# Performance work log

Hardware: AMD Instinct MI355X
Metric: run time of the kernel (lower is better)

The kernel has to match this reference:

```python
import jax, jax.numpy as jnp
import numpy as np
from jax.scipy.special import gammaln

NEARZERO = 1e-5
LENF = 15  # gamma unit-hydrograph length (days)

# (name, low, high) in the exact order of Exphydro.parameter_bounds
PHY_BOUNDS = [
    ('ddf', 0.0, 40.0), ('Tbm', -2.0, 3.0), ('wrf', 0.0, 0.5), ('Tbf', -5.0, 2.0),
    ('Kf', 0.0, 5.0), ('exp_fe', 0.0, 1.0), ('ET_efficiency', 0.0, 1.0),
    ('coef_runoff', 0.0, 1.0), ('coef_vadose2phreatic', 1e-5, 0.02),
    ('coef_vadose', 0.0, 0.1), ('coef_phreatic', 1e-5, 0.01),
    ('vadose_max_level', 1e-3, 500.0)]
ROUT_BOUNDS = [('alpha1', 0.3, 20.0), ('beta1', 0.01, 5.0),
               ('alpha2', 0.5, 13.0), ('beta2', 0.15, 1.5)]


def setup_inputs() -> dict:
    key = jax.random.key(0)
    k1, k2, k3, k4 = jax.random.split(key, 4)
    T, G = 1095, 15000
    prcp = jax.random.uniform(k1, (T, G), dtype=jnp.float32) * 10.0   # mm/day
    tmean = jax.random.normal(k2, (T, G), dtype=jnp.float32) * 10.0   # deg C (spans <0 and >0)
    pet = jax.random.uniform(k3, (T, G), dtype=jnp.float32) * 5.0     # mm/day
    x_phy = jnp.stack([prcp, tmean, pet], axis=-1)                    # [T, G, 3]
    params = jax.random.uniform(k4, (G, 16), dtype=jnp.float32)       # normalized in [0,1]
    return {'x_phy': x_phy, 'params': params}


def _descale(p, lo, hi):
    # change_param_range: linear rescale of [0,1]-normalized params
    return p * (hi - lo) + lo


def _uh_gamma(alpha, theta, lenF=LENF):
    # Gamma-pdf unit hydrograph, normalized. alpha, theta: [G] -> w: [lenF, G]
    t = jnp.arange(lenF, dtype=alpha.dtype) + 0.5          # midpoint of each day
    a = alpha[None, :]
    th = theta[None, :]
    logw = (a - 1.0) * jnp.log(t[:, None]) - t[:, None] / th - gammaln(a) - a * jnp.log(th)
    w = jnp.exp(logw)
    return w / jnp.sum(w, axis=0, keepdims=True)


def _uh_conv(q, w):
    # causal depthwise convolution along time. q: [T, G], w: [L, G]
    T = q.shape[0]
    L = w.shape[0]
    qp = jnp.pad(q, ((L - 1, 0), (0, 0)))
    out = jnp.zeros_like(q)
    for l in range(L):  # fixed small L=15, unrolled at trace time
        out = out + w[l][None, :] * qp[L - 1 - l:L - 1 - l + T]
    return out


def _forward(x_phy, params):
    G = params.shape[0]
    # unpack + descale: 12 static physical params [G,1] (nmul=1), 4 routing params [G]
    phy = {name: _descale(params[:, i:i + 1], lo, hi)
           for i, (name, lo, hi) in enumerate(PHY_BOUNDS)}
    rout = {name: _descale(params[:, 12 + i], lo, hi)
            for i, (name, lo, hi) in enumerate(ROUT_BOUNDS)}

    P = x_phy[..., 0:1]    # [T, G, 1] precip
    Tm = x_phy[..., 1:2]   # [T, G, 1] mean temperature
    Pet = x_phy[..., 2:3]  # [T, G, 1] potential ET

    def step(carry, inp):
        sog, wis, vad, phr = carry  # snow-on-ground, water-in-snowpack, vadose, phreatic [G,1]
        p, tm, pet = inp
        rain = p * (tm >= 0.0).astype(p.dtype)
        snow = p * (tm < 0.0).astype(p.dtype)
        # overnight refreezing of liquid water in snowpack
        pot_freeze = phy['Kf'] * jnp.clip(phy['Tbf'] - tm, NEARZERO, None) ** phy['exp_fe']
        freeze = jnp.minimum(pot_freeze, wis)
        wis = wis - freeze
        sog = sog + freeze
        # degree-day snowmelt
        melt = jnp.minimum(jnp.clip(phy['ddf'] * (tm - phy['Tbm']), 0.0, None), sog + snow)
        sog = sog + snow - melt
        # snowpack liquid retention
        retention = phy['wrf'] * sog
        wtmp = wis + melt + rain
        avail = jnp.clip(wtmp - retention, 0.0, None)
        wis = jnp.where(avail > 0.0, retention, wtmp)
        # soil buckets
        ret_pot = phy['ET_efficiency'] * pet
        ratio = vad / phy['vadose_max_level']
        ht0 = phy['coef_runoff'] * ratio * avail                 # surface runoff
        infil = avail - ht0
        ht1 = phy['coef_vadose2phreatic'] * ratio * vad          # vadose -> phreatic
        ht2 = phy['coef_vadose'] * vad                           # delayed runoff (interflow)
        ht3 = phy['coef_phreatic'] * phr                         # baseflow
        aet = jnp.minimum(ret_pot, vad)                          # actual ET
        vad = vad + infil - aet - ht1 - ht2
        overflow = jnp.clip(vad - phy['vadose_max_level'], 0.0, None)
        vad = jnp.clip(vad, NEARZERO, phy['vadose_max_level'])
        ht0 = ht0 + overflow
        phr = jnp.clip(phr + ht1 - ht3, NEARZERO, None)
        return (sog, wis, vad, phr), (ht0, ht2, ht3, aet, vad, phr)

    init = tuple(jnp.full((G, 1), NEARZERO, dtype=x_phy.dtype) for _ in range(4))
    _, (ht0, ht2, ht3, aet, vad_sim, phr_sim) = jax.lax.scan(step, init, (P, Tm, Pet))

    # average over nmul (muwts=None, nmul=1) -> [T, G]
    q_surf = jnp.mean(ht0, axis=-1)
    q_delay = jnp.mean(ht2 + ht3, axis=-1)
    # gamma unit-hydrograph routing
    uh1 = _uh_gamma(rout['alpha1'], rout['beta1'])
    uh2 = _uh_gamma(rout['alpha2'], rout['beta2'])
    return _uh_conv(q_surf, uh1) + _uh_conv(q_delay, uh2)  # streamflow [T, G]


def reference(x_phy, params):
    return _forward(x_phy, params)
```

## Files before the change

kernel.cpp:

```cpp
#include <hip/hip_runtime.h>

#define LENF 15
#define NZ   1e-5f

typedef float f32x2 __attribute__((ext_vector_type(2)));

struct R3 { float p, t, e; };

__global__ __launch_bounds__(64, 1) void exphydro_kernel(
    const float* __restrict__ x,
    const float* __restrict__ params,
    float* __restrict__ out,
    int G, int T)
{
  int g = blockIdx.x * 64 + threadIdx.x;
  if (g >= G) return;

  const float* pp = params + (size_t)g * 16;
  float P0[16];
#pragma unroll
  for (int i = 0; i < 16; ++i) P0[i] = pp[i];

  const float ddf    = P0[0]  * 40.f;
  const float Tbm    = P0[1]  * 5.f  - 2.f;
  const float wrf    = P0[2]  * 0.5f;
  const float Tbf    = P0[3]  * 7.f  - 5.f;
  const float Kf     = P0[4]  * 5.f;
  const float exp_fe = P0[5];
  const float ET_eff = P0[6];
  const float c_vad  = P0[9]  * 0.1f;
  const float c_phr  = P0[10] * (0.01f - 1e-5f) + 1e-5f;
  const float vml    = P0[11] * (500.f - 0.001f) + 0.001f;
  const float inv_vml = 1.f / vml;
  const float crp    = P0[7] * inv_vml;
  const float cvp    = (P0[8] * (0.02f - 1e-5f) + 1e-5f) * inv_vml;
  const float mpb    = ddf * Tbm;
  const float a1     = P0[12] * (20.f - 0.3f)  + 0.3f;
  const float b1     = P0[13] * (5.f  - 0.01f) + 0.01f;
  const float a2     = P0[14] * (13.f - 0.5f)  + 0.5f;
  const float b2     = P0[15] * (1.5f - 0.15f) + 0.15f;

  f32x2 wv[LENF];
  {
    float lw1[LENF], lw2[LENF];
    float m1 = -1e30f, m2 = -1e30f;
    const float ib1 = 1.f / b1, ib2 = 1.f / b2;
#pragma unroll
    for (int l = 0; l < LENF; ++l) {
      float tt = l + 0.5f;
      float lt = __logf(tt);
      lw1[l] = (a1 - 1.f) * lt - tt * ib1;
      lw2[l] = (a2 - 1.f) * lt - tt * ib2;
      m1 = fmaxf(m1, lw1[l]);
      m2 = fmaxf(m2, lw2[l]);
    }
    float s1 = 0.f, s2 = 0.f;
    float t1[LENF], t2[LENF];
#pragma unroll
    for (int l = 0; l < LENF; ++l) {
      t1[l] = __expf(lw1[l] - m1); s1 += t1[l];
      t2[l] = __expf(lw2[l] - m2); s2 += t2[l];
    }
    const float r1 = 1.f / s1, r2 = 1.f / s2;
#pragma unroll
    for (int l = 0; l < LENF; ++l) { wv[l].x = t1[l] * r1; wv[l].y = t2[l] * r2; }
  }

  float sog = NZ, wis = NZ, vad = NZ, phr = NZ;
  f32x2 D[LENF - 1];
#pragma unroll
  for (int l = 0; l < LENF - 1; ++l) D[l] = (f32x2){0.f, 0.f};

  const unsigned Gu = (unsigned)G;
  const R3* xg = (const R3*)x + g;
  unsigned oof = (unsigned)g;

  R3 A[LENF], B[LENF];
  float pf[LENF], mp[LENF], rp[LENF];

  const int nb   = T / LENF;
  const int tail = T - nb * LENF;

#define LOAD(BUF, blk)                                                \
  {                                                                   \
    unsigned b0_ = (unsigned)(blk) * (unsigned)LENF * Gu;             \
    _Pragma("unroll")                                                 \
    for (int j = 0; j < LENF; ++j) BUF[j] = xg[b0_ + (unsigned)j * Gu]; \
  }

#define PREP(BUF)                                                     \
  {                                                                   \
    _Pragma("unroll")                                                 \
    for (int j = 0; j < LENF; ++j) {                                  \
      float tm_ = BUF[j].t;                                           \
      pf[j] = Kf * __builtin_amdgcn_exp2f(                            \
                  exp_fe * __builtin_amdgcn_logf(fmaxf(Tbf - tm_, NZ))); \
      mp[j] = fmaxf(ddf * tm_ - mpb, 0.f);                            \
      rp[j] = ET_eff * BUF[j].e;                                      \
    }                                                                 \
  }

#define STEP(BUF, I_)                                                 \
  {                                                                   \
    float p_ = BUF[I_].p, tm_ = BUF[I_].t;                            \
    float rain = (tm_ >= 0.f) ? p_ : 0.f;                             \
    float snow = p_ - rain;                                           \
    float freeze = fminf(pf[I_], wis);                                \
    wis -= freeze;                                                    \
    float sos = sog + freeze + snow;                                  \
    float melt = fminf(mp[I_], sos);                                  \
    sog = sos - melt;                                                 \
    float ret = wrf * sog;                                            \
    float wtmp = wis + melt + rain;                                   \
    float avail = fmaxf(wtmp - ret, 0.f);                             \
    wis = fminf(wtmp, ret);              \
    float t1_ = crp * vad;                                            \
    float ht0 = t1_ * avail;                                          \
    float t2_ = cvp * vad;                                            \
    float ht1 = t2_ * vad;                                            \
    float ht2 = c_vad * vad;                                          \
    float ht3 = c_phr * phr;                                          \
    float infil = avail - ht0;                                        \
    float aet = fminf(rp[I_], vad);                                   \
    float va_ = vad + infil;                                          \
    float vb_ = aet + ht1;                                            \
    float v2_ = va_ - vb_ - ht2;                                      \
    float overflow = fmaxf(v2_ - vml, 0.f);                           \
    vad = fminf(fmaxf(v2_, NZ), vml);                 \
    float qx = ht0 + overflow;                                        \
    phr = fmaxf(phr + ht1 - ht3, NZ);                                 \
    f32x2 q_; q_.x = qx; q_.y = ht2 + ht3;                            \
    f32x2 o_ = D[0] + wv[0] * q_;                                     \
    _Pragma("unroll")                                                 \
    for (int l = 0; l < LENF - 2; ++l)                                \
      D[l] = D[l + 1] + wv[l + 1] * q_;             \
    D[LENF - 2] = wv[LENF - 1] * q_;                                  \
    out[oof] = o_.x + o_.y;                                           \
    oof += Gu;                                                        \
  }

#define BLOCK(BUF)                                                    \
  {                                                                   \
    PREP(BUF);                                                        \
    _Pragma("unroll")                                                 \
    for (int i = 0; i < LENF; ++i) STEP(BUF, i);                      \
  }

  if (nb > 0) LOAD(A, 0);

  int k = 0;
  while (k + 2 <= nb) {
    LOAD(B, k + 1);
    BLOCK(A);
    if (k + 2 < nb) LOAD(A, k + 2);
    BLOCK(B);
    k += 2;
  }
  if (k < nb) {
    BLOCK(A);
  }
  if (tail > 0) {
    unsigned b0 = (unsigned)nb * (unsigned)LENF * Gu;
    for (int j = 0; j < tail; ++j) {
      A[0] = xg[b0 + (unsigned)j * Gu];
      float tm_ = A[0].t;
      pf[0] = Kf * __builtin_amdgcn_exp2f(
                  exp_fe * __builtin_amdgcn_logf(fmaxf(Tbf - tm_, NZ)));
      mp[0] = fmaxf(ddf * tm_ - mpb, 0.f);
      rp[0] = ET_eff * A[0].e;
      STEP(A, 0);
    }
  }

#undef LOAD
#undef PREP
#undef STEP
#undef BLOCK
}

extern "C" void kernel_launch(void* const* d_in, const int* in_sizes, int n_in,
                              void* d_out, int out_size, void* d_ws, size_t ws_size,
                              hipStream_t stream) {
  const float* x      = (const float*)d_in[0];
  const float* params = (const float*)d_in[1];
  float* out          = (float*)d_out;

  int G = in_sizes[1] / 16;
  int T = in_sizes[0] / (G * 3);

  int block = 64;
  int grid  = (G + block - 1) / block;
  exphydro_kernel<<<grid, block, 0, stream>>>(x, params, out, G, T);
}
```

Before: 149.5 us.

## Software-pipeline snow and soil phases across time chunks to expose ILP

Splits each serial time step into a snow/melt phase and a soil/routing phase. The soil phase of chunk k-1 is interleaved with the snow phase of chunk k, which are independent, so the latency-bound recurrence has two dependency chains in flight. It also cuts the input chunk from 15 to 5 steps, double-buffered, and replaces the tail path with clamped loads and guarded counts. The shorter prefetch distance may hide memory latency less well, and the extra avail/rp arrays add register pressure.

```diff
diff --git a/kernel.cpp b/kernel.cpp
--- a/kernel.cpp
+++ b/kernel.cpp
@@ -1,6 +1,7 @@
 #include <hip/hip_runtime.h>
 
 #define LENF 15
+#define BLK  5
 #define NZ   1e-5f
 
 typedef float f32x2 __attribute__((ext_vector_type(2)));
@@ -66,7 +67,8 @@
     for (int l = 0; l < LENF; ++l) { wv[l].x = t1[l] * r1; wv[l].y = t2[l] * r2; }
   }
 
-  float sog = NZ, wis = NZ, vad = NZ, phr = NZ;
+  float sog = NZ, wis = NZ;
+  float vad = NZ, phr = NZ;
   f32x2 D[LENF - 1];
 #pragma unroll
   for (int l = 0; l < LENF - 1; ++l) D[l] = (f32x2){0.f, 0.f};
@@ -74,57 +76,67 @@
   const unsigned Gu = (unsigned)G;
   const R3* xg = (const R3*)x + g;
   unsigned oof = (unsigned)g;
-
-  R3 A[LENF], B[LENF];
-  float pf[LENF], mp[LENF], rp[LENF];
-
-  const int nb   = T / LENF;
-  const int tail = T - nb * LENF;
-
-#define LOAD(BUF, blk)                                                \
-  {                                                                   \
-    unsigned b0_ = (unsigned)(blk) * (unsigned)LENF * Gu;             \
-    _Pragma("unroll")                                                 \
-    for (int j = 0; j < LENF; ++j) BUF[j] = xg[b0_ + (unsigned)j * Gu]; \
-  }
-
-#define PREP(BUF)                                                     \
-  {                                                                   \
-    _Pragma("unroll")                                                 \
-    for (int j = 0; j < LENF; ++j) {                                  \
-      float tm_ = BUF[j].t;                                           \
-      pf[j] = Kf * __builtin_amdgcn_exp2f(                            \
-                  exp_fe * __builtin_amdgcn_logf(fmaxf(Tbf - tm_, NZ))); \
-      mp[j] = fmaxf(ddf * tm_ - mpb, 0.f);                            \
-      rp[j] = ET_eff * BUF[j].e;                                      \
+  const unsigned tmax = (unsigned)(T - 1);
+
+  R3 XA[BLK], XB[BLK];
+  float pf[BLK], mp[BLK];
+  float avail[BLK], rp[BLK];
+
+  const int nc = (T + BLK - 1) / BLK;
+
+#define LOADC(BUF, c)                                                 \
+  {                                                                   \
+    unsigned tb_ = (unsigned)(c) * (unsigned)BLK;                     \
+    _Pragma("unroll")                                                 \
+    for (int j = 0; j < BLK; ++j) {                                   \
+      unsigned t_ = tb_ + (unsigned)j;                                \
+      if (t_ > tmax) t_ = tmax;                                       \
+      BUF[j] = xg[t_ * Gu];                                           \
     }                                                                 \
   }
 
-#define STEP(BUF, I_)                                                 \
-  {                                                                   \
-    float p_ = BUF[I_].p, tm_ = BUF[I_].t;                            \
+#define PREPC(BUF, cnt)                                               \
+  {                                                                   \
+    _Pragma("unroll")                                                 \
+    for (int j = 0; j < BLK; ++j) {                                   \
+      if (j < (cnt)) {                                                \
+        float tm_ = BUF[j].t;                                         \
+        pf[j] = Kf * __builtin_amdgcn_exp2f(                          \
+            exp_fe * __builtin_amdgcn_logf(fmaxf(Tbf - tm_, NZ)));    \
+        mp[j] = fmaxf(ddf * tm_ - mpb, 0.f);                          \
+      }                                                               \
+    }                                                                 \
+  }
+
+#define P1STEP(BUF, J_)                                               \
+  {                                                                   \
+    float p_ = BUF[J_].p, tm_ = BUF[J_].t;                            \
     float rain = (tm_ >= 0.f) ? p_ : 0.f;                             \
     float snow = p_ - rain;                                           \
-    float freeze = fminf(pf[I_], wis);                                \
+    float freeze = fminf(pf[J_], wis);                                \
     wis -= freeze;                                                    \
     float sos = sog + freeze + snow;                                  \
-    float melt = fminf(mp[I_], sos);                                  \
+    float melt = fminf(mp[J_], sos);                                  \
     sog = sos - melt;                                                 \
     float ret = wrf * sog;                                            \
     float wtmp = wis + melt + rain;                                   \
-    float avail = fmaxf(wtmp - ret, 0.f);                             \
+    avail[J_] = fmaxf(wtmp - ret, 0.f);                               \
     wis = fminf(wtmp, ret);              \
+    rp[J_] = ET_eff * BUF[J_].e;                                      \
+  }
+
+#define P2STEP(J_)                                                    \
+  {                                                                   \
+    float av_ = avail[J_], rp_ = rp[J_];                              \
     float t1_ = crp * vad;                                            \
-    float ht0 = t1_ * avail;                                          \
+    float ht0 = t1_ * av_;                                            \
     float t2_ = cvp * vad;                                            \
     float ht1 = t2_ * vad;                                            \
     float ht2 = c_vad * vad;                                          \
     float ht3 = c_phr * phr;                                          \
-    float infil = avail - ht0;                                        \
-    float aet = fminf(rp[I_], vad);                                   \
-    float va_ = vad + infil;                                          \
-    float vb_ = aet + ht1;                                            \
-    float v2_ = va_ - vb_ - ht2;                                      \
+    float infil = av_ - ht0;                                          \
+    float aet = fminf(rp_, vad);                                      \
+    float v2_ = vad + infil - aet - ht1 - ht2;                        \
     float overflow = fmaxf(v2_ - vml, 0.f);                           \
     vad = fminf(fmaxf(v2_, NZ), vml);                 \
     float qx = ht0 + overflow;                                        \
@@ -139,43 +151,52 @@
     oof += Gu;                                                        \
   }
 
-#define BLOCK(BUF)                                                    \
-  {                                                                   \
-    PREP(BUF);                                                        \
-    _Pragma("unroll")                                                 \
-    for (int i = 0; i < LENF; ++i) STEP(BUF, i);                      \
-  }
-
-  if (nb > 0) LOAD(A, 0);
-
-  int k = 0;
-  while (k + 2 <= nb) {
-    LOAD(B, k + 1);
-    BLOCK(A);
-    if (k + 2 < nb) LOAD(A, k + 2);
-    BLOCK(B);
+#define CHUNK(BUF, p1cnt, p2cnt)                                      \
+  {                                                                   \
+    PREPC(BUF, p1cnt);                                                \
+    _Pragma("unroll")                                                 \
+    for (int j = 0; j < BLK; ++j) {                                   \
+      if (j < (p2cnt)) P2STEP(j);                                     \
+      if (j < (p1cnt)) P1STEP(BUF, j);                                \
+    }                                                                 \
+  }
+
+  if (nc > 0) LOADC(XA, 0);
+  if (nc > 1) LOADC(XB, 1);
+  {
+    int c0 = (T < BLK) ? T : BLK;
+    PREPC(XA, c0);
+#pragma unroll
+    for (int j = 0; j < BLK; ++j) if (j < c0) P1STEP(XA, j);
+  }
+
+  int k = 1;
+  while ((k + 2) * BLK <= T) {
+    LOADC(XA, k + 1);
+    CHUNK(XB, BLK, BLK);
+    if (k + 2 < nc) LOADC(XB, k + 2);
+    CHUNK(XA, BLK, BLK);
     k += 2;
   }
-  if (k < nb) {
-    BLOCK(A);
-  }
-  if (tail > 0) {
-    unsigned b0 = (unsigned)nb * (unsigned)LENF * Gu;
-    for (int j = 0; j < tail; ++j) {
-      A[0] = xg[b0 + (unsigned)j * Gu];
-      float tm_ = A[0].t;
-      pf[0] = Kf * __builtin_amdgcn_exp2f(
-                  exp_fe * __builtin_amdgcn_logf(fmaxf(Tbf - tm_, NZ)));
-      mp[0] = fmaxf(ddf * tm_ - mpb, 0.f);
-      rp[0] = ET_eff * A[0].e;
-      STEP(A, 0);
+  while (k < nc) {
+    if (k + 1 < nc) {
+      if ((k + 1) & 1) { LOADC(XB, k + 1); } else { LOADC(XA, k + 1); }
     }
-  }
-
-#undef LOAD
-#undef PREP
-#undef STEP
-#undef BLOCK
+    int p1c = T - k * BLK; if (p1c > BLK) p1c = BLK;
+    if (k & 1) { CHUNK(XB, p1c, BLK); } else { CHUNK(XA, p1c, BLK); }
+    ++k;
+  }
+  {
+    int p2c = T - (nc - 1) * BLK;
+#pragma unroll
+    for (int j = 0; j < BLK; ++j) if (j < p2c) P2STEP(j);
+  }
+
+#undef LOADC
+#undef PREPC
+#undef P1STEP
+#undef P2STEP
+#undef CHUNK
 }
 
 extern "C" void kernel_launch(void* const* d_in, const int* in_sizes, int n_in,
```

Measured after the change: 193.7 us. +29.6%, slower.

## Split recurrence and UH convolution into separate kernels with bf16 intermediate

Applied to the files above, without the earlier changes.

Splits the fused per-basin kernel into three launches. A weights kernel computes the unit-hydrograph weights. A recurrence kernel writes the two runoff components packed as bf16 into workspace. A time-tiled convolution kernel with 256-thread blocks runs the 15-tap filter in parallel across time chunks. The aim is to take the convolution and its register pressure off the serial critical path and to expose more parallelism than 235 single-wave blocks give. The cost is extra launches, a workspace memset and round-trip traffic to the intermediate buffer, and storing intermediates in bf16 lowers precision. The recurrence step is also algebraically rearranged to shorten its dependency chain.

```diff
diff --git a/kernel.cpp b/kernel.cpp
--- a/kernel.cpp
+++ b/kernel.cpp
@@ -2,25 +2,225 @@
 
 #define LENF 15
 #define NZ   1e-5f
+#define TT   120
 
 typedef float f32x2 __attribute__((ext_vector_type(2)));
 
 struct R3 { float p, t, e; };
 
-__global__ __launch_bounds__(64, 1) void exphydro_kernel(
+__device__ __forceinline__ void uh_weights(float a, float b, float* w) {
+  float lw[LENF], m = -1e30f;
+  const float ib = 1.f / b;
+#pragma unroll
+  for (int l = 0; l < LENF; ++l) {
+    float tt = l + 0.5f;
+    lw[l] = (a - 1.f) * __logf(tt) - tt * ib;
+    m = fmaxf(m, lw[l]);
+  }
+  float s = 0.f;
+#pragma unroll
+  for (int l = 0; l < LENF; ++l) { w[l] = __expf(lw[l] - m); s += w[l]; }
+  const float r = 1.f / s;
+#pragma unroll
+  for (int l = 0; l < LENF; ++l) w[l] *= r;
+}
+
+__global__ __launch_bounds__(64, 1) void k_weights(
+    const float* __restrict__ params, f32x2* __restrict__ wv, int G)
+{
+  int g = blockIdx.x * 64 + threadIdx.x;
+  if (g >= G) return;
+  const float* pp = params + (size_t)g * 16;
+  float w1[LENF], w2[LENF];
+  uh_weights(pp[12] * (20.f - 0.3f) + 0.3f, pp[13] * (5.f - 0.01f) + 0.01f, w1);
+  uh_weights(pp[14] * (13.f - 0.5f) + 0.5f, pp[15] * (1.5f - 0.15f) + 0.15f, w2);
+#pragma unroll
+  for (int l = 0; l < LENF; ++l)
+    wv[(size_t)l * G + g] = (f32x2){w1[l], w2[l]};
+}
+
+__global__ __launch_bounds__(64, 1) void k_recur(
     const float* __restrict__ x,
     const float* __restrict__ params,
+    unsigned* __restrict__ qp,
+    int G, int T)
+{
+  int g = blockIdx.x * 64 + threadIdx.x;
+  const int gs = (g < G) ? g : (G - 1);
+
+  const float* pp = params + (size_t)gs * 16;
+  const float ddf    = pp[0]  * 40.f;
+  const float Tbm    = pp[1]  * 5.f  - 2.f;
+  const float wrf    = pp[2]  * 0.5f;
+  const float Tbf    = pp[3]  * 7.f  - 5.f;
+  const float Kf     = pp[4]  * 5.f;
+  const float exp_fe = pp[5];
+  const float ET_eff = pp[6];
+  const float c_vad  = pp[9]  * 0.1f;
+  const float c_phr  = pp[10] * (0.01f - 1e-5f) + 1e-5f;
+  const float vml    = pp[11] * (500.f - 0.001f) + 0.001f;
+  const float inv_vml = 1.f / vml;
+  const float crp    = pp[7] * inv_vml;
+  const float cvp    = (pp[8] * (0.02f - 1e-5f) + 1e-5f) * inv_vml;
+  const float mpb    = ddf * Tbm;
+  const float omcp   = 1.f - c_phr;
+
+  float sog = NZ, wis = NZ, vad = NZ, phr = NZ;
+
+  const unsigned Gu = (unsigned)G;
+  const R3* xg = (const R3*)x + gs;
+  unsigned oof = 14u * Gu + (unsigned)gs;
+
+  R3 A[LENF], B[LENF];
+  float px[LENF], snmp[LENF], pf[LENF], rp[LENF];
+  const int nb = T / LENF;
+
+#define LOAD(BUF, blk)                                                \
+  {                                                                   \
+    unsigned b0_ = (unsigned)(blk) * (unsigned)LENF * Gu;             \
+    _Pragma("unroll")                                                 \
+    for (int j = 0; j < LENF; ++j) BUF[j] = xg[b0_ + (unsigned)j * Gu]; \
+  }
+
+#define PREP(BUF)                                                     \
+  {                                                                   \
+    _Pragma("unroll")                                                 \
+    for (int j = 0; j < LENF; ++j) {                                  \
+      float p_ = BUF[j].p, tm_ = BUF[j].t;                            \
+      float rain_ = (tm_ >= 0.f) ? p_ : 0.f;                          \
+      float mp_ = fmaxf(ddf * tm_ - mpb, 0.f);                        \
+      px[j]   = p_;                                                   \
+      snmp[j] = (p_ - rain_) - mp_;                                   \
+      pf[j]   = Kf * __builtin_amdgcn_exp2f(                          \
+          exp_fe * __builtin_amdgcn_logf(fmaxf(Tbf - tm_, NZ)));      \
+      rp[j]   = ET_eff * BUF[j].e;                                    \
+    }                                                                 \
+  }
+
+#define STEPJ(J_)                                                     \
+  {                                                                   \
+    float freeze = fminf(pf[J_], wis);                                \
+    float sg_ = sog + snmp[J_];                                       \
+    float sog2 = fmaxf(sg_ + freeze, 0.f);                            \
+    float base = (wis + sog) + px[J_];                                \
+    float wtmp = base - sog2;                                         \
+    float ret = wrf * sog2;                                           \
+    float avail = fmaxf(wtmp - ret, 0.f);                             \
+    wis = fminf(wtmp, ret);                                           \
+    sog = sog2;                                                       \
+    float t2v = cvp * vad;                                            \
+    float u_  = t2v + c_vad;                                          \
+    float h12 = u_ * vad;                                             \
+    float aet = fminf(rp[J_], vad);                                   \
+    float K1 = (vad - aet) - h12;                                     \
+    float C  = crp * vad;                                             \
+    float ht1 = t2v * vad;                                            \
+    float ht2 = c_vad * vad;                                          \
+    float tv = K1 + avail;                                            \
+    float v2 = fmaf(-C, avail, tv);                                   \
+    float overflow = fmaxf(v2 - vml, 0.f);                            \
+    vad = fminf(fmaxf(v2, NZ), vml);                      \
+    float qx = fmaf(C, avail, overflow);                              \
+    float qd = fmaf(c_phr, phr, ht2);                                 \
+    phr = fmaxf(fmaf(phr, omcp, ht1), NZ);                            \
+    unsigned pk_;                                                     \
+    asm("v_cvt_pk_bf16_f32 %0, %1, %2" : "=v"(pk_) : "v"(qx), "v"(qd)); \
+    qp[oof] = pk_;                                                    \
+    oof += Gu;                                                        \
+  }
+
+#define BLOCKC(BUF)                                                   \
+  {                                                                   \
+    PREP(BUF);                                                        \
+    _Pragma("unroll")                                                 \
+    for (int j = 0; j < LENF; ++j) STEPJ(j);                          \
+  }
+
+  LOAD(A, 0);
+  int k = 0;
+  while (k + 2 <= nb) {
+    LOAD(B, k + 1);
+    BLOCKC(A);
+    if (k + 2 < nb) LOAD(A, k + 2);
+    BLOCKC(B);
+    k += 2;
+  }
+  if (k < nb) { BLOCKC(A); }
+  for (int t = nb * LENF; t < T; ++t) {
+    R3 r = xg[(unsigned)t * Gu];
+    float rain_ = (r.t >= 0.f) ? r.p : 0.f;
+    px[0] = r.p;
+    snmp[0] = (r.p - rain_) - fmaxf(ddf * r.t - mpb, 0.f);
+    pf[0] = Kf * __builtin_amdgcn_exp2f(
+        exp_fe * __builtin_amdgcn_logf(fmaxf(Tbf - r.t, NZ)));
+    rp[0] = ET_eff * r.e;
+    STEPJ(0);
+  }
+#undef LOAD
+#undef PREP
+#undef STEPJ
+#undef BLOCKC
+}
+
+__global__ __launch_bounds__(256, 2) void k_conv(
+    const unsigned* __restrict__ qp,
+    const f32x2* __restrict__ wv,
     float* __restrict__ out,
     int G, int T)
 {
+  const int g  = blockIdx.x * 256 + threadIdx.x;
+  const int gs = (g < G) ? g : (G - 1);
+  const int t0 = blockIdx.y * TT;
+  const int steps = min(TT, T - t0);
+  const int nch = steps / LENF;
+  const unsigned Gu = (unsigned)G;
+
+  f32x2 w[LENF];
+#pragma unroll
+  for (int l = 0; l < LENF; ++l) w[l] = wv[(size_t)l * Gu + gs];
+
+  const unsigned* qb = qp + (size_t)t0 * Gu + gs;
+
+  f32x2 r[LENF];
+#pragma unroll
+  for (int j = 0; j < LENF - 1; ++j) {
+    unsigned u = qb[(size_t)j * Gu];
+    r[j].x = __uint_as_float(u << 16);
+    r[j].y = __uint_as_float(u & 0xFFFF0000u);
+  }
+
+  float* ob = out + (size_t)t0 * Gu + gs;
+  const bool valid = (g < G);
+
+  for (int cc = 0; cc < nch; ++cc) {
+    const size_t rb = (size_t)(cc * LENF + 14) * Gu;
+#pragma unroll
+    for (int m = 0; m < LENF; ++m) {
+      const int slot = (m + 14) % LENF;
+      unsigned u = qb[rb + (size_t)m * Gu];
+      r[slot].x = __uint_as_float(u << 16);
+      r[slot].y = __uint_as_float(u & 0xFFFF0000u);
+      f32x2 acc = (f32x2){0.f, 0.f};
+#pragma unroll
+      for (int l = 0; l < LENF; ++l) {
+        const int s = (m + 14 - l + LENF) % LENF;
+        acc += w[l] * r[s];
+      }
+      if (valid) ob[(size_t)(cc * LENF + m) * Gu] = acc.x + acc.y;
+    }
+  }
+}
+
+__global__ __launch_bounds__(64, 1) void exphydro_fused(
+    const float* __restrict__ x, const float* __restrict__ params,
+    float* __restrict__ out, int G, int T)
+{
   int g = blockIdx.x * 64 + threadIdx.x;
   if (g >= G) return;
-
   const float* pp = params + (size_t)g * 16;
   float P0[16];
 #pragma unroll
   for (int i = 0; i < 16; ++i) P0[i] = pp[i];
-
   const float ddf    = P0[0]  * 40.f;
   const float Tbm    = P0[1]  * 5.f  - 2.f;
   const float wrf    = P0[2]  * 0.5f;
@@ -35,85 +235,49 @@
   const float crp    = P0[7] * inv_vml;
   const float cvp    = (P0[8] * (0.02f - 1e-5f) + 1e-5f) * inv_vml;
   const float mpb    = ddf * Tbm;
-  const float a1     = P0[12] * (20.f - 0.3f)  + 0.3f;
-  const float b1     = P0[13] * (5.f  - 0.01f) + 0.01f;
-  const float a2     = P0[14] * (13.f - 0.5f)  + 0.5f;
-  const float b2     = P0[15] * (1.5f - 0.15f) + 0.15f;
-
   f32x2 wv[LENF];
   {
-    float lw1[LENF], lw2[LENF];
-    float m1 = -1e30f, m2 = -1e30f;
-    const float ib1 = 1.f / b1, ib2 = 1.f / b2;
-#pragma unroll
-    for (int l = 0; l < LENF; ++l) {
-      float tt = l + 0.5f;
-      float lt = __logf(tt);
-      lw1[l] = (a1 - 1.f) * lt - tt * ib1;
-      lw2[l] = (a2 - 1.f) * lt - tt * ib2;
-      m1 = fmaxf(m1, lw1[l]);
-      m2 = fmaxf(m2, lw2[l]);
-    }
-    float s1 = 0.f, s2 = 0.f;
-    float t1[LENF], t2[LENF];
-#pragma unroll
-    for (int l = 0; l < LENF; ++l) {
-      t1[l] = __expf(lw1[l] - m1); s1 += t1[l];
-      t2[l] = __expf(lw2[l] - m2); s2 += t2[l];
-    }
-    const float r1 = 1.f / s1, r2 = 1.f / s2;
-#pragma unroll
-    for (int l = 0; l < LENF; ++l) { wv[l].x = t1[l] * r1; wv[l].y = t2[l] * r2; }
-  }
-
+    float w1[LENF], w2[LENF];
+    uh_weights(P0[12] * (20.f - 0.3f) + 0.3f, P0[13] * (5.f - 0.01f) + 0.01f, w1);
+    uh_weights(P0[14] * (13.f - 0.5f) + 0.5f, P0[15] * (1.5f - 0.15f) + 0.15f, w2);
+#pragma unroll
+    for (int l = 0; l < LENF; ++l) wv[l] = (f32x2){w1[l], w2[l]};
+  }
   float sog = NZ, wis = NZ, vad = NZ, phr = NZ;
   f32x2 D[LENF - 1];
 #pragma unroll
   for (int l = 0; l < LENF - 1; ++l) D[l] = (f32x2){0.f, 0.f};
-
   const unsigned Gu = (unsigned)G;
   const R3* xg = (const R3*)x + g;
   unsigned oof = (unsigned)g;
-
   R3 A[LENF], B[LENF];
   float pf[LENF], mp[LENF], rp[LENF];
-
-  const int nb   = T / LENF;
-  const int tail = T - nb * LENF;
-
-#define LOAD(BUF, blk)                                                \
-  {                                                                   \
-    unsigned b0_ = (unsigned)(blk) * (unsigned)LENF * Gu;             \
-    _Pragma("unroll")                                                 \
-    for (int j = 0; j < LENF; ++j) BUF[j] = xg[b0_ + (unsigned)j * Gu]; \
-  }
-
-#define PREP(BUF)                                                     \
-  {                                                                   \
-    _Pragma("unroll")                                                 \
+  const int nb = T / LENF;
+#define LOADF(BUF, blk)                                               \
+  { unsigned b0_ = (unsigned)(blk) * (unsigned)LENF * Gu;             \
+    _Pragma("unroll")                                                 \
+    for (int j = 0; j < LENF; ++j) BUF[j] = xg[b0_ + (unsigned)j * Gu]; }
+#define PREPF(BUF)                                                    \
+  { _Pragma("unroll")                                                 \
     for (int j = 0; j < LENF; ++j) {                                  \
       float tm_ = BUF[j].t;                                           \
       pf[j] = Kf * __builtin_amdgcn_exp2f(                            \
-                  exp_fe * __builtin_amdgcn_logf(fmaxf(Tbf - tm_, NZ))); \
+          exp_fe * __builtin_amdgcn_logf(fmaxf(Tbf - tm_, NZ)));      \
       mp[j] = fmaxf(ddf * tm_ - mpb, 0.f);                            \
-      rp[j] = ET_eff * BUF[j].e;                                      \
-    }                                                                 \
-  }
-
-#define STEP(BUF, I_)                                                 \
-  {                                                                   \
-    float p_ = BUF[I_].p, tm_ = BUF[I_].t;                            \
+      rp[j] = ET_eff * BUF[j].e; } }
+#define STEPF(BUF, J_)                                                \
+  { float p_ = BUF[J_].p, tm_ = BUF[J_].t;                            \
     float rain = (tm_ >= 0.f) ? p_ : 0.f;                             \
     float snow = p_ - rain;                                           \
-    float freeze = fminf(pf[I_], wis);                                \
+    float freeze = fminf(pf[J_], wis);                                \
     wis -= freeze;                                                    \
     float sos = sog + freeze + snow;                                  \
-    float melt = fminf(mp[I_], sos);                                  \
+    float melt = fminf(mp[J_], sos);                                  \
     sog = sos - melt;                                                 \
     float ret = wrf * sog;                                            \
     float wtmp = wis + melt + rain;                                   \
     float avail = fmaxf(wtmp - ret, 0.f);                             \
-    wis = fminf(wtmp, ret);              \
+    wis = fminf(wtmp, ret);                                           \
     float t1_ = crp * vad;                                            \
     float ht0 = t1_ * avail;                                          \
     float t2_ = cvp * vad;                                            \
@@ -121,61 +285,41 @@
     float ht2 = c_vad * vad;                                          \
     float ht3 = c_phr * phr;                                          \
     float infil = avail - ht0;                                        \
-    float aet = fminf(rp[I_], vad);                                   \
-    float va_ = vad + infil;                                          \
-    float vb_ = aet + ht1;                                            \
-    float v2_ = va_ - vb_ - ht2;                                      \
+    float aet = fminf(rp[J_], vad);                                   \
+    float v2_ = vad + infil - aet - ht1 - ht2;                        \
     float overflow = fmaxf(v2_ - vml, 0.f);                           \
-    vad = fminf(fmaxf(v2_, NZ), vml);                 \
+    vad = fminf(fmaxf(v2_, NZ), vml);                                 \
     float qx = ht0 + overflow;                                        \
     phr = fmaxf(phr + ht1 - ht3, NZ);                                 \
     f32x2 q_; q_.x = qx; q_.y = ht2 + ht3;                            \
     f32x2 o_ = D[0] + wv[0] * q_;                                     \
     _Pragma("unroll")                                                 \
     for (int l = 0; l < LENF - 2; ++l)                                \
-      D[l] = D[l + 1] + wv[l + 1] * q_;             \
+      D[l] = D[l + 1] + wv[l + 1] * q_;                               \
     D[LENF - 2] = wv[LENF - 1] * q_;                                  \
     out[oof] = o_.x + o_.y;                                           \
-    oof += Gu;                                                        \
-  }
-
-#define BLOCK(BUF)                                                    \
-  {                                                                   \
-    PREP(BUF);                                                        \
-    _Pragma("unroll")                                                 \
-    for (int i = 0; i < LENF; ++i) STEP(BUF, i);                      \
-  }
-
-  if (nb > 0) LOAD(A, 0);
-
+    oof += Gu; }
+  LOADF(A, 0);
   int k = 0;
   while (k + 2 <= nb) {
-    LOAD(B, k + 1);
-    BLOCK(A);
-    if (k + 2 < nb) LOAD(A, k + 2);
-    BLOCK(B);
+    LOADF(B, k + 1);
+    PREPF(A);
+#pragma unroll
+    for (int j = 0; j < LENF; ++j) STEPF(A, j);
+    if (k + 2 < nb) LOADF(A, k + 2);
+    PREPF(B);
+#pragma unroll
+    for (int j = 0; j < LENF; ++j) STEPF(B, j);
     k += 2;
   }
   if (k < nb) {
-    BLOCK(A);
-  }
-  if (tail > 0) {
-    unsigned b0 = (unsigned)nb * (unsigned)LENF * Gu;
-    for (int j = 0; j < tail; ++j) {
-      A[0] = xg[b0 + (unsigned)j * Gu];
-      float tm_ = A[0].t;
-      pf[0] = Kf * __builtin_amdgcn_exp2f(
-                  exp_fe * __builtin_amdgcn_logf(fmaxf(Tbf - tm_, NZ)));
-      mp[0] = fmaxf(ddf * tm_ - mpb, 0.f);
-      rp[0] = ET_eff * A[0].e;
-      STEP(A, 0);
-    }
-  }
-
-#undef LOAD
-#undef PREP
-#undef STEP
-#undef BLOCK
+    PREPF(A);
+#pragma unroll
+    for (int j = 0; j < LENF; ++j) STEPF(A, j);
+  }
+#undef LOADF
+#undef PREPF
+#undef STEPF
 }
 
 extern "C" void kernel_launch(void* const* d_in, const int* in_sizes, int n_in,
@@ -188,7 +332,20 @@
   int G = in_sizes[1] / 16;
   int T = in_sizes[0] / (G * 3);
 
-  int block = 64;
-  int grid  = (G + block - 1) / block;
-  exphydro_kernel<<<grid, block, 0, stream>>>(x, params, out, G, T);
-}
+  size_t qBytes = (size_t)(T + 14) * G * 4;
+  size_t wBytes = (size_t)G * LENF * 8;
+
+  if (ws_size >= qBytes + wBytes && (T % LENF) == 0) {
+    unsigned* qp = (unsigned*)d_ws;
+    f32x2*    wv = (f32x2*)((char*)d_ws + qBytes);
+    hipMemsetAsync(d_ws, 0, (size_t)14 * G * 4, stream);
+    int grid64 = (G + 63) / 64;
+    k_weights<<<grid64, 64, 0, stream>>>(params, wv, G);
+    k_recur<<<grid64, 64, 0, stream>>>(x, params, qp, G, T);
+    dim3 g2((G + 255) / 256, (T + TT - 1) / TT);
+    k_conv<<<g2, 256, 0, stream>>>(qp, wv, out, G, T);
+  } else {
+    int grid64 = (G + 63) / 64;
+    exphydro_fused<<<grid64, 64, 0, stream>>>(x, params, out, G, T);
+  }
+}
```

Result: slower. 192.1 us (+28.5%).
